# Performance work log

Measured on AMD Instinct MI355X. Metric: run time of the kernel, lower is better.

## Reference

```python
import jax, jax.numpy as jnp
import numpy as np

B, S, E, H, TOP = 256, 200, 64, 128, 200
LOC, T, N, HEADS, ALPHA = 50000, 168, 5000, 3, 0.2
NEG = -9e15


def _position_encoding(time_number, n_units, f=100.0):
    pos = np.arange(time_number, dtype=np.float32)
    unit = np.arange(n_units // 2, dtype=np.float32)
    rad = pos[None, :] / (f ** (unit[:, None] / (n_units // 2)))
    emb = np.concatenate([np.sin(rad), np.cos(rad)], axis=0)  # [n_units, T]
    return jnp.asarray(emb.T)  # [T, n_units]


def setup_inputs():
    key = jax.random.key(0)
    ks = jax.random.split(key, 24)
    inp = {}
    inp['u1'] = jax.random.randint(ks[0], (B,), 0, N)
    inp['u2'] = jax.random.randint(ks[1], (B,), 0, N)
    inp['length_1'] = jax.random.randint(ks[2], (B,), 2, S + 1)
    inp['length_2'] = jax.random.randint(ks[3], (B,), 2, S + 1)
    inp['loc_1'] = jax.random.randint(ks[4], (B, S), 0, LOC + 1)
    inp['loc_2'] = jax.random.randint(ks[5], (B, S), 0, LOC + 1)
    inp['time_1'] = jax.random.randint(ks[6], (B, S), 0, T)
    inp['time_2'] = jax.random.randint(ks[7], (B, S), 0, T)
    inp['time_gap_1'] = jax.random.uniform(ks[8], (B, S), jnp.float32) * 2.0
    inp['time_gap_2'] = jax.random.uniform(ks[9], (B, S), jnp.float32) * 2.0
    # parameters
    inp['loc_emb'] = jax.random.normal(ks[10], (LOC + 1, E), jnp.float32)
    inp['time_emb'] = _position_encoding(T, E, 100.0)  # frozen
    inp['user_emb'] = jax.random.normal(ks[11], (N, E), jnp.float32)
    g = 1.414 * jnp.sqrt(6.0 / (E + E))
    inp['gat_W'] = jax.random.uniform(ks[12], (HEADS, E, E), jnp.float32, -g, g)
    ga = 1.414 * jnp.sqrt(6.0 / (2 * E + 1))
    inp['gat_a'] = jax.random.uniform(ks[13], (HEADS, 2 * E, 1), jnp.float32, -ga, ga)
    inp['gat_Wout'] = jax.random.uniform(ks[14], (E, E), jnp.float32, -g, g)
    inp['gat_aout'] = jax.random.uniform(ks[15], (2 * E, 1), jnp.float32, -ga, ga)
    adj = (jax.random.uniform(ks[16], (N, N)) < 0.01).astype(jnp.float32)
    inp['adj'] = jnp.maximum(adj, jnp.eye(N, dtype=jnp.float32))
    s = 1.0 / jnp.sqrt(H)
    inp['Wih'] = jax.random.uniform(ks[17], (4 * H, E), jnp.float32, -s, s)
    inp['Whh'] = jax.random.uniform(ks[18], (4 * H, H), jnp.float32, -s, s)
    inp['bih'] = jax.random.uniform(ks[19], (4 * H,), jnp.float32, -s, s)
    inp['bhh'] = jax.random.uniform(ks[20], (4 * H,), jnp.float32, -s, s)
    inp['time_v'] = jax.random.uniform(ks[21], (H, 1), jnp.float32, -0.1, 0.1)
    inp['time_w'] = jnp.full((1, 1), 0.05, jnp.float32)
    inp['time_b'] = jnp.full((1, 1), 0.02, jnp.float32)
    fin = 2 * TOP + H + E
    sf = 1.0 / jnp.sqrt(fin)
    inp['fc_w'] = jax.random.uniform(ks[22], (2, fin), jnp.float32, -sf, sf)
    inp['fc_b'] = jax.random.uniform(ks[23], (2,), jnp.float32, -sf, sf)
    return inp


def _lstm(x, Wih, Whh, bih, bhh):
    # x: [B, S, E] -> hidden states [B, S, H], torch gate order i,f,g,o
    b = x.shape[0]
    xg = jnp.einsum('bse,ge->bsg', x, Wih) + bih + bhh  # [B,S,4H]

    def step(carry, xt):
        h, c = carry
        g = xt + h @ Whh.T
        i, f, gg, o = jnp.split(g, 4, axis=-1)
        c = jax.nn.sigmoid(f) * c + jax.nn.sigmoid(i) * jnp.tanh(gg)
        h = jax.nn.sigmoid(o) * jnp.tanh(c)
        return (h, c), h

    init = (jnp.zeros((b, H), x.dtype), jnp.zeros((b, H), x.dtype))
    _, hs = jax.lax.scan(step, init, xg.transpose(1, 0, 2))
    return hs.transpose(1, 0, 2)


def _gat_layer(x, W, a, adj):
    h = x @ W  # [N,F]
    F = h.shape[1]
    f1 = h @ a[:F, 0]  # [N]
    f2 = h @ a[F:, 0]  # [N]
    e = jax.nn.leaky_relu(f1[:, None] + f2[None, :], ALPHA)
    att = jnp.where(adj > 0, e, NEG)
    att = jax.nn.softmax(att, axis=1)
    return jax.nn.elu(att @ h)


def _gat(x, adj, gat_W, gat_a, gat_Wout, gat_aout):
    temp = jnp.zeros((x.shape[0], E), x.dtype)
    for i in range(HEADS):
        temp = temp + _gat_layer(x, gat_W[i], gat_a[i], adj)
    return _gat_layer(temp / HEADS, gat_Wout, gat_aout, adj)


def _time_loss(length, hidden, time_gap, time_v, time_w, time_b):
    tg = jnp.concatenate([time_gap[:, 1:], jnp.zeros((time_gap.shape[0], 1), time_gap.dtype)], axis=-1)
    p1 = jnp.einsum('bsh,h->bs', hidden, time_v[:, 0])
    w, bb = time_w[0, 0], time_b[0, 0]
    p2 = w * tg
    p3 = (1.0 / w) * jnp.exp(p1 + bb)
    p4 = (1.0 / w) * jnp.exp(p1 + p2 + bb)
    f1 = p1 + p2 + bb + p3 - p4  # [B,S]
    mask = jnp.arange(S)[None, :] < (length - 1)[:, None]
    per = jnp.sum(jnp.where(mask, f1, 0.0), axis=1) / (length - 1).astype(f1.dtype)
    return -jnp.mean(per)


def _masked_cos_vec(cos, length_1, length_2):
    # cos: [B,S,S]; row-max over valid cols, col-max over valid rows, zero-padded
    idx = jnp.arange(S)
    colm = idx[None, None, :] < length_2[:, None, None]
    rowm = idx[None, :, None] < length_1[:, None, None]
    hang = jnp.max(jnp.where(colm, cos, -jnp.inf), axis=2)  # [B,S]
    hang = jnp.where(idx[None, :] < length_1[:, None], hang, 0.0)
    lie = jnp.max(jnp.where(rowm, cos, -jnp.inf), axis=1)  # [B,S]
    lie = jnp.where(idx[None, :] < length_2[:, None], lie, 0.0)
    return jnp.concatenate([hang, lie], axis=1)  # [B, 2*TOP]


def reference(time_gap_1, time_gap_2, loc_emb, time_emb, user_emb, gat_W, gat_a,
              gat_Wout, gat_aout, adj, Wih, Whh, bih, bhh, time_v, time_w, time_b,
              fc_w, fc_b, u1, u2, length_1, length_2, loc_1, loc_2, time_1, time_2):
    # cosine-similarity matrix
    le1 = loc_emb[loc_1]  # [B,S,E]
    le2 = loc_emb[loc_2]
    n1 = jnp.sqrt(jnp.sum(le1 ** 2, axis=2))  # [B,S]
    n2 = jnp.sqrt(jnp.sum(le2 ** 2, axis=2))
    cos = jnp.einsum('bse,bte->bst', le1, le2) / (n1[:, :, None] * n2[:, None, :])
    matrix_ans = _masked_cos_vec(cos, length_1, length_2)

    # temporal LSTM branch (dropout inactive in eval)
    te1 = time_emb[time_1]
    te2 = time_emb[time_2]
    h1 = _lstm(te1, Wih, Whh, bih, bhh)
    h2 = _lstm(te2, Wih, Whh, bih, bhh)
    loss1 = _time_loss(length_1, h1, time_gap_1, time_v, time_w, time_b)
    loss2 = _time_loss(length_2, h2, time_gap_2, time_v, time_w, time_b)
    time_loss = loss1 + loss2

    bidx = jnp.arange(h1.shape[0])
    seq1 = h1[bidx, length_1 - 1]  # [B,H]
    seq2 = h2[bidx, length_2 - 1]
    time_ans = seq1 * seq2

    # GAT user embeddings (get_gat over full user graph)
    gat_embedding = _gat(user_emb, adj, gat_W, gat_a, gat_Wout, gat_aout)
    u_hadamard = gat_embedding[u1] * gat_embedding[u2]

    feat = jnp.concatenate([matrix_ans, jnp.tanh(time_ans), jnp.tanh(u_hadamard)], axis=1)
    outs = feat @ fc_w.T + fc_b
    return outs, time_loss
```

## Files before the change

### kernel.cpp

```cpp
#include <hip/hip_runtime.h>
#include <math.h>

#define Bb 256
#define Ss 200
#define Ee 64
#define Hh 128
#define Nn 5000
#define MAXN 160

__device__ __forceinline__ float wredsum(float v){
  #pragma unroll
  for (int o = 32; o; o >>= 1) v += __shfl_xor(v, o);
  return v;
}
__device__ __forceinline__ float wredmax(float v){
  #pragma unroll
  for (int o = 32; o; o >>= 1) v = fmaxf(v, __shfl_xor(v, o));
  return v;
}
__device__ __forceinline__ float sigf(float x){ return 1.f / (1.f + __expf(-x)); }
__device__ __forceinline__ float tanh_f(float x){
  float e = __expf(-2.f * fabsf(x));
  float t = (1.f - e) / (1.f + e);
  return copysignf(t, x);
}

__global__ void norm_gather(const float* __restrict__ loc_emb,
                            const int* __restrict__ loc1, const int* __restrict__ loc2,
                            float* __restrict__ ne1, float* __restrict__ ne2){
  int wid = blockIdx.x * 4 + (threadIdx.x >> 6);
  int lane = threadIdx.x & 63;
  const int total = Bb * Ss;
  if (wid >= 2 * total) return;
  const int* loc = (wid < total) ? loc1 : loc2;
  float* ne = (wid < total) ? ne1 : ne2;
  int r = (wid < total) ? wid : wid - total;
  int idx = loc[r];
  float v = loc_emb[(size_t)idx * Ee + lane];
  float ss = wredsum(v * v);
  ne[(size_t)r * Ee + lane] = v * rsqrtf(ss);
}

__global__ __launch_bounds__(256) void cosmax_kernel(const float* __restrict__ ne1,
                                                     const float* __restrict__ ne2,
                                                     const int* __restrict__ len1,
                                                     const int* __restrict__ len2,
                                                     float* __restrict__ matrix_ans){
  __shared__ __align__(16) float As[128][68];
  __shared__ __align__(16) float Bs[128][68];
  int b = blockIdx.x, tid = threadIdx.x;
  int tx = tid & 15, ty = tid >> 4;
  int L1 = len1[b], L2 = len2[b];
  const float4 zero4 = make_float4(0.f, 0.f, 0.f, 0.f);
  float lie[16];
  #pragma unroll
  for (int i = 0; i < 16; i++) lie[i] = -3.0e38f;

  for (int sc = 0; sc < 2; sc++){
    float hang[8];
    #pragma unroll
    for (int i = 0; i < 8; i++) hang[i] = -3.0e38f;
    __syncthreads();
    for (int i = tid; i < 2048; i += 256){
      int r = i >> 4, kq = i & 15;
      int row = sc * 128 + r;
      float4 v = (row < Ss) ? ((const float4*)ne1)[((size_t)b * Ss + row) * 16 + kq] : zero4;
      *(float4*)&As[r][kq * 4] = v;
    }
    for (int tc = 0; tc < 2; tc++){
      __syncthreads();
      for (int i = tid; i < 2048; i += 256){
        int r = i >> 4, kq = i & 15;
        int col = tc * 128 + r;
        float4 v = (col < Ss) ? ((const float4*)ne2)[((size_t)b * Ss + col) * 16 + kq] : zero4;
        *(float4*)&Bs[r][kq * 4] = v;
      }
      __syncthreads();
      float acc[8][8];
      #pragma unroll
      for (int i = 0; i < 8; i++)
        #pragma unroll
        for (int j = 0; j < 8; j++) acc[i][j] = 0.f;
      #pragma unroll 4
      for (int k4 = 0; k4 < 16; k4++){
        float4 a4[8], b4[8];
        #pragma unroll
        for (int i = 0; i < 8; i++) a4[i] = *(const float4*)&As[ty + 16 * i][k4 * 4];
        #pragma unroll
        for (int j = 0; j < 8; j++) b4[j] = *(const float4*)&Bs[tx + 16 * j][k4 * 4];
        #pragma unroll
        for (int i = 0; i < 8; i++)
          #pragma unroll
          for (int j = 0; j < 8; j++)
            acc[i][j] += a4[i].x * b4[j].x + a4[i].y * b4[j].y
                       + a4[i].z * b4[j].z + a4[i].w * b4[j].w;
      }
      #pragma unroll
      for (int j = 0; j < 8; j++){
        int col = tc * 128 + tx + 16 * j;
        bool cv = col < L2;
        #pragma unroll
        for (int i = 0; i < 8; i++){
          int row = sc * 128 + ty + 16 * i;
          float v = acc[i][j];
          if (cv) hang[i] = fmaxf(hang[i], v);
          if (row < L1) lie[tc * 8 + j] = fmaxf(lie[tc * 8 + j], v);
        }
      }
    }
    __syncthreads();
    float* fl = &As[0][0];
    #pragma unroll
    for (int i = 0; i < 8; i++) fl[(ty + 16 * i) * 16 + tx] = hang[i];
    __syncthreads();
    if (tid < 128){
      float m = -3.0e38f;
      #pragma unroll
      for (int p = 0; p < 16; p++) m = fmaxf(m, fl[tid * 16 + p]);
      int row = sc * 128 + tid;
      if (row < Ss) matrix_ans[(size_t)b * 400 + row] = (row < L1) ? m : 0.f;
    }
  }
  __syncthreads();
  float* fl = &As[0][0];
  #pragma unroll
  for (int i = 0; i < 16; i++){
    int tcc = i >> 3, j = i & 7;
    fl[(tcc * 128 + tx + 16 * j) * 16 + ty] = lie[i];
  }
  __syncthreads();
  {
    int t = tid;
    float m = -3.0e38f;
    #pragma unroll
    for (int p = 0; p < 16; p++) m = fmaxf(m, fl[t * 16 + p]);
    if (t < Ss) matrix_ans[(size_t)b * 400 + 200 + t] = (t < L2) ? m : 0.f;
  }
}

__global__ void xg_table(const float* __restrict__ time_emb, const float* __restrict__ Wih,
                         const float* __restrict__ bih, const float* __restrict__ bhh,
                         float* __restrict__ xgtab){
  int tt = blockIdx.x, g = threadIdx.x;
  __shared__ float xs[64];
  if (g < 64) xs[g] = time_emb[tt * 64 + g];
  __syncthreads();
  float acc = bih[g] + bhh[g];
  #pragma unroll
  for (int k = 0; k < 64; k++) acc += Wih[g * 64 + k] * xs[k];
  xgtab[tt * 512 + g] = acc;
}

__global__ __launch_bounds__(512) void lstm_kernel(const float* __restrict__ xgtab,
                                                   const int* __restrict__ time_1,
                                                   const int* __restrict__ time_2,
                                                   const float* __restrict__ Whh,
                                                   const float* __restrict__ tg1,
                                                   const float* __restrict__ tg2,
                                                   const int* __restrict__ len1,
                                                   const int* __restrict__ len2,
                                                   const float* __restrict__ time_v,
                                                   const float* __restrict__ time_w,
                                                   const float* __restrict__ time_b,
                                                   float* __restrict__ hfin1,
                                                   float* __restrict__ hfin2,
                                                   float* __restrict__ perb){
  int b = blockIdx.x, g = threadIdx.x;
  int lane = g & 63;
  __shared__ __align__(16) float h1s[128], h2s[128];
  __shared__ float g1s[512], g2s[512];
  __shared__ int t1s[Ss], t2s[Ss];
  __shared__ float tgs[2][Ss];
  __shared__ float red[4];
  float4 w4[32];
  #pragma unroll
  for (int k = 0; k < 32; k++) w4[k] = *(const float4*)(Whh + (size_t)g * 128 + k * 4);
  for (int i = g; i < Ss; i += 512){
    t1s[i] = time_1[b * Ss + i];
    t2s[i] = time_2[b * Ss + i];
    tgs[0][i] = (i < Ss - 1) ? tg1[b * Ss + i + 1] : 0.f;
    tgs[1][i] = (i < Ss - 1) ? tg2[b * Ss + i + 1] : 0.f;
  }
  if (g < 128){ h1s[g] = 0.f; h2s[g] = 0.f; }
  int l1 = len1[b], l2 = len2[b];
  float wv = time_w[0], bbias = time_b[0];
  float iw = 1.f / wv;
  float vd = (g < 256) ? time_v[g & 127] : 0.f;
  float lacc = 0.f;
  float c_reg = 0.f;
  __syncthreads();
  for (int t = 0; t < Ss; t++){
    float xg1 = xgtab[t1s[t] * 512 + g];
    float xg2 = xgtab[t2s[t] * 512 + g];
    float a1a = 0.f, a1b = 0.f, a2a = 0.f, a2b = 0.f;
    #pragma unroll
    for (int k = 0; k < 32; k += 2){
      float4 ha0 = *(const float4*)&h1s[k * 4];
      float4 hb0 = *(const float4*)&h2s[k * 4];
      float4 ha1 = *(const float4*)&h1s[k * 4 + 4];
      float4 hb1 = *(const float4*)&h2s[k * 4 + 4];
      a1a += w4[k].x * ha0.x + w4[k].y * ha0.y + w4[k].z * ha0.z + w4[k].w * ha0.w;
      a2a += w4[k].x * hb0.x + w4[k].y * hb0.y + w4[k].z * hb0.z + w4[k].w * hb0.w;
      a1b += w4[k+1].x * ha1.x + w4[k+1].y * ha1.y + w4[k+1].z * ha1.z + w4[k+1].w * ha1.w;
      a2b += w4[k+1].x * hb1.x + w4[k+1].y * hb1.y + w4[k+1].z * hb1.z + w4[k+1].w * hb1.w;
    }
    g1s[g] = a1a + a1b + xg1;
    g2s[g] = a2a + a2b + xg2;
    __syncthreads();
    if (g < 256){
      int d = g & 127;
      const float* gs = (g < 128) ? g1s : g2s;
      float ii = sigf(gs[d]);
      float ff = sigf(gs[128 + d]);
      float gg = tanh_f(gs[256 + d]);
      float oo = sigf(gs[384 + d]);
      float c = ff * c_reg + ii * gg;
      c_reg = c;
      float h = oo * tanh_f(c);
      if (g < 128){ h1s[d] = h; if (t == l1 - 1) hfin1[(size_t)b * 128 + d] = h; }
      else        { h2s[d] = h; if (t == l2 - 1) hfin2[(size_t)b * 128 + d] = h; }
      float r = wredsum(h * vd);
      if (lane == 0) red[g >> 6] = r;
    }
    __syncthreads();
    if (g < 2){
      float p = (g == 0) ? (red[0] + red[1]) : (red[2] + red[3]);
      int L = (g == 0) ? l1 : l2;
      if (t < L - 1){
        float p2 = wv * tgs[g][t];
        lacc += p + p2 + bbias + iw * expf(p + bbias) - iw * expf(p + p2 + bbias);
      }
    }
  }
  if (g < 2) red[g] = lacc;
  __syncthreads();
  if (g == 0) perb[b] = red[0] / (float)(l1 - 1) + red[1] / (float)(l2 - 1);
}

__global__ void build_csr(const float* __restrict__ adj, int* __restrict__ nbr, int* __restrict__ deg){
  int row = blockIdx.x * 4 + (threadIdx.x >> 6);
  int lane = threadIdx.x & 63;
  if (row >= Nn) return;
  const float* ar = adj + (size_t)row * Nn;
  int cnt = 0;
  for (int base = 0; base < Nn; base += 64){
    int c = base + lane;
    bool nz = (c < Nn) && (ar[c] > 0.f);
    unsigned long long m = __ballot(nz);
    if (nz){
      int pos = cnt + __popcll(m & ((1ULL << lane) - 1ULL));
      if (pos < MAXN) nbr[(size_t)row * MAXN + pos] = c;
    }
    cnt += __popcll(m);
  }
  if (lane == 0) deg[row] = (cnt > MAXN) ? MAXN : cnt;
}

__global__ __launch_bounds__(256) void gat_xw(const float* __restrict__ x, float scale,
                                              const float* __restrict__ W,
                                              const float* __restrict__ avec,
                                              float* __restrict__ hmat,
                                              float* __restrict__ f1, float* __restrict__ f2){
  __shared__ float Ws[64][64];
  __shared__ float as_[128];
  __shared__ float xs[4][64];
  int tid = threadIdx.x, lane = tid & 63, wid = tid >> 6;
  for (int i = tid; i < 4096; i += 256) Ws[i >> 6][i & 63] = W[i];
  if (tid < 128) as_[tid] = avec[tid];
  __syncthreads();
  int row = blockIdx.x * 4 + wid;
  xs[wid][lane] = x[(size_t)row * 64 + lane] * scale;
  float acc = 0.f;
  #pragma unroll
  for (int k = 0; k < 64; k++) acc += xs[wid][k] * Ws[k][lane];
  float p1 = wredsum(acc * as_[lane]);
  float p2 = wredsum(acc * as_[64 + lane]);
  hmat[(size_t)row * 64 + lane] = acc;
  if (lane == 0){ f1[row] = p1; f2[row] = p2; }
}

__global__ __launch_bounds__(256) void gat_att(const float* __restrict__ hmat,
                                               const float* __restrict__ f1,
                                               const float* __restrict__ f2,
                                               const int* __restrict__ nbr,
                                               const int* __restrict__ deg,
                                               float* __restrict__ outp, int accum){
  __shared__ int nbs[4][MAXN];
  __shared__ float attb[4][MAXN];
  int tid = threadIdx.x, lane = tid & 63, w = tid >> 6;
  int row = blockIdx.x * 4 + w;
  int d = deg[row];
  float fr = f1[row];
  float mx = -3.0e38f;
  for (int j = lane; j < d; j += 64){
    int c = nbr[(size_t)row * MAXN + j];
    nbs[w][j] = c;
    float e = fr + f2[c];
    e = (e >= 0.f) ? e : 0.2f * e;
    attb[w][j] = e;
    mx = fmaxf(mx, e);
  }
  mx = wredmax(mx);
  float sum = 0.f;
  for (int j = lane; j < d; j += 64){
    float ex = __expf(attb[w][j] - mx);
    attb[w][j] = ex;
    sum += ex;
  }
  sum = wredsum(sum);
  float inv = 1.f / sum;
  float acc = 0.f;
  for (int j = 0; j < d; j++)
    acc += attb[w][j] * hmat[(size_t)nbs[w][j] * 64 + lane];
  acc *= inv;
  acc = (acc > 0.f) ? acc : expm1f(acc);
  if (accum) outp[(size_t)row * 64 + lane] += acc;
  else       outp[(size_t)row * 64 + lane] = acc;
}

__global__ void final_fc(const float* __restrict__ matrix_ans,
                         const float* __restrict__ hfin1, const float* __restrict__ hfin2,
                         const float* __restrict__ gat_emb,
                         const int* __restrict__ u1, const int* __restrict__ u2,
                         const float* __restrict__ fc_w, const float* __restrict__ fc_b,
                         const float* __restrict__ perb, float* __restrict__ out){
  int b = blockIdx.x, lane = threadIdx.x;
  int a = u1[b], c = u2[b];
  float acc0 = 0.f, acc1 = 0.f;
  for (int i = lane; i < 592; i += 64){
    float f;
    if (i < 400) f = matrix_ans[(size_t)b * 400 + i];
    else if (i < 528){
      int d = i - 400;
      f = tanhf(hfin1[(size_t)b * 128 + d] * hfin2[(size_t)b * 128 + d]);
    } else {
      int d = i - 528;
      f = tanhf(gat_emb[(size_t)a * 64 + d] * gat_emb[(size_t)c * 64 + d]);
    }
    acc0 += f * fc_w[i];
    acc1 += f * fc_w[592 + i];
  }
  acc0 = wredsum(acc0);
  acc1 = wredsum(acc1);
  if (lane == 0){
    out[b * 2]     = acc0 + fc_b[0];
    out[b * 2 + 1] = acc1 + fc_b[1];
  }
  if (b == 0){
    float ls = 0.f;
    for (int i = lane; i < 256; i += 64) ls += perb[i];
    ls = wredsum(ls);
    if (lane == 0) out[512] = -ls / 256.f;
  }
}

extern "C" void kernel_launch(void* const* d_in, const int* in_sizes, int n_in,
                              void* d_out, int out_size, void* d_ws, size_t ws_size,
                              hipStream_t stream){
  (void)in_sizes; (void)n_in; (void)out_size; (void)ws_size;
  const int*   u1       = (const int*)  d_in[0];
  const int*   u2       = (const int*)  d_in[1];
  const int*   len1     = (const int*)  d_in[2];
  const int*   len2     = (const int*)  d_in[3];
  const int*   loc1     = (const int*)  d_in[4];
  const int*   loc2     = (const int*)  d_in[5];
  const int*   time1    = (const int*)  d_in[6];
  const int*   time2    = (const int*)  d_in[7];
  const float* tg1      = (const float*)d_in[8];
  const float* tg2      = (const float*)d_in[9];
  const float* loc_emb  = (const float*)d_in[10];
  const float* time_emb = (const float*)d_in[11];
  const float* user_emb = (const float*)d_in[12];
  const float* gat_W    = (const float*)d_in[13];
  const float* gat_a    = (const float*)d_in[14];
  const float* gat_Wout = (const float*)d_in[15];
  const float* gat_aout = (const float*)d_in[16];
  const float* adj      = (const float*)d_in[17];
  const float* Wih      = (const float*)d_in[18];
  const float* Whh      = (const float*)d_in[19];
  const float* bih      = (const float*)d_in[20];
  const float* bhh      = (const float*)d_in[21];
  const float* time_v   = (const float*)d_in[22];
  const float* time_w   = (const float*)d_in[23];
  const float* time_b   = (const float*)d_in[24];
  const float* fc_w     = (const float*)d_in[25];
  const float* fc_b     = (const float*)d_in[26];
  float* out = (float*)d_out;

  size_t off = 0;
  auto alloc = [&](size_t nbytes) -> void* {
    void* p = (char*)d_ws + off;
    off += (nbytes + 255) & ~(size_t)255;
    return p;
  };
  float* ne1        = (float*)alloc((size_t)Bb * Ss * Ee * 4);
  float* ne2        = (float*)alloc((size_t)Bb * Ss * Ee * 4);
  float* matrix_ans = (float*)alloc((size_t)Bb * 400 * 4);
  float* xgtab      = (float*)alloc((size_t)168 * 512 * 4);
  float* hfin1      = (float*)alloc((size_t)Bb * Hh * 4);
  float* hfin2      = (float*)alloc((size_t)Bb * Hh * 4);
  float* gat_h      = (float*)alloc((size_t)Nn * 64 * 4);
  float* gat_acc    = (float*)alloc((size_t)Nn * 64 * 4);
  float* gat_emb    = (float*)alloc((size_t)Nn * 64 * 4);
  float* f1w        = (float*)alloc((size_t)Nn * 4);
  float* f2w        = (float*)alloc((size_t)Nn * 4);
  float* perb       = (float*)alloc((size_t)Bb * 4);
  int*   nbr        = (int*)  alloc((size_t)Nn * MAXN * 4);
  int*   deg        = (int*)  alloc((size_t)Nn * 4);

  norm_gather<<<(2 * Bb * Ss) / 4, 256, 0, stream>>>(loc_emb, loc1, loc2, ne1, ne2);
  cosmax_kernel<<<Bb, 256, 0, stream>>>(ne1, ne2, len1, len2, matrix_ans);

  xg_table<<<168, 512, 0, stream>>>(time_emb, Wih, bih, bhh, xgtab);
  lstm_kernel<<<Bb, 512, 0, stream>>>(xgtab, time1, time2, Whh, tg1, tg2, len1, len2,
                                      time_v, time_w, time_b, hfin1, hfin2, perb);

  build_csr<<<Nn / 4, 256, 0, stream>>>(adj, nbr, deg);
  for (int hd = 0; hd < 3; hd++){
    gat_xw<<<Nn / 4, 256, 0, stream>>>(user_emb, 1.f, gat_W + (size_t)hd * 64 * 64,
                                       gat_a + (size_t)hd * 128, gat_h, f1w, f2w);
    gat_att<<<Nn / 4, 256, 0, stream>>>(gat_h, f1w, f2w, nbr, deg, gat_acc, hd == 0 ? 0 : 1);
  }
  gat_xw<<<Nn / 4, 256, 0, stream>>>(gat_acc, 1.f / 3.f, gat_Wout, gat_aout, gat_h, f1w, f2w);
  gat_att<<<Nn / 4, 256, 0, stream>>>(gat_h, f1w, f2w, nbr, deg, gat_emb, 0);

  final_fc<<<Bb, 64, 0, stream>>>(matrix_ans, hfin1, hfin2, gat_emb,
                                  u1, u2, fc_w, fc_b, perb, out);
}
```

Measured before the change: 909.6 us.

## Split LSTM recurrent matvec across lane quarters with 4 gates per thread

```diff
diff --git a/kernel.cpp b/kernel.cpp
--- a/kernel.cpp
+++ b/kernel.cpp
@@ -151,37 +151,43 @@
   xgtab[tt * 512 + g] = acc;
 }
 
-__global__ __launch_bounds__(512) void lstm_kernel(const float* __restrict__ xgtab,
-                                                   const int* __restrict__ time_1,
-                                                   const int* __restrict__ time_2,
-                                                   const float* __restrict__ Whh,
-                                                   const float* __restrict__ tg1,
-                                                   const float* __restrict__ tg2,
-                                                   const int* __restrict__ len1,
-                                                   const int* __restrict__ len2,
-                                                   const float* __restrict__ time_v,
-                                                   const float* __restrict__ time_w,
-                                                   const float* __restrict__ time_b,
-                                                   float* __restrict__ hfin1,
-                                                   float* __restrict__ hfin2,
-                                                   float* __restrict__ perb){
+#define HIDX(d) ((d) + (((d) >> 5) << 2))
+__global__ __launch_bounds__(512, 2) void lstm_kernel(const float* __restrict__ xgtab,
+                                                      const int* __restrict__ time_1,
+                                                      const int* __restrict__ time_2,
+                                                      const float* __restrict__ Whh,
+                                                      const float* __restrict__ tg1,
+                                                      const float* __restrict__ tg2,
+                                                      const int* __restrict__ len1,
+                                                      const int* __restrict__ len2,
+                                                      const float* __restrict__ time_v,
+                                                      const float* __restrict__ time_w,
+                                                      const float* __restrict__ time_b,
+                                                      float* __restrict__ hfin1,
+                                                      float* __restrict__ hfin2,
+                                                      float* __restrict__ perb){
   int b = blockIdx.x, g = threadIdx.x;
-  int lane = g & 63;
-  __shared__ __align__(16) float h1s[128], h2s[128];
-  __shared__ float g1s[512], g2s[512];
+  int lane = g & 63, wave = g >> 6;
+  int kq = lane >> 4;
+  int g0 = (wave * 16 + (lane & 15)) * 4;
+  __shared__ __align__(16) float h1s[144], h2s[144];
+  __shared__ __align__(16) float g1s[512], g2s[512];
   __shared__ int t1s[Ss], t2s[Ss];
   __shared__ float tgs[2][Ss];
   __shared__ float red[4];
-  float4 w4[32];
-  #pragma unroll
-  for (int k = 0; k < 32; k++) w4[k] = *(const float4*)(Whh + (size_t)g * 128 + k * 4);
+  float4 w4[4][8];
+  #pragma unroll
+  for (int j = 0; j < 4; j++)
+    #pragma unroll
+    for (int q = 0; q < 8; q++)
+      w4[j][q] = *(const float4*)(Whh + (size_t)(g0 + j) * 128 + kq * 32 + q * 4);
   for (int i = g; i < Ss; i += 512){
     t1s[i] = time_1[b * Ss + i];
     t2s[i] = time_2[b * Ss + i];
     tgs[0][i] = (i < Ss - 1) ? tg1[b * Ss + i + 1] : 0.f;
     tgs[1][i] = (i < Ss - 1) ? tg2[b * Ss + i + 1] : 0.f;
   }
-  if (g < 128){ h1s[g] = 0.f; h2s[g] = 0.f; }
+  if (g < 144){ h1s[g] = 0.f; h2s[g] = 0.f; }
   int l1 = len1[b], l2 = len2[b];
   float wv = time_w[0], bbias = time_b[0];
   float iw = 1.f / wv;
@@ -190,22 +196,36 @@
   float c_reg = 0.f;
   __syncthreads();
   for (int t = 0; t < Ss; t++){
-    float xg1 = xgtab[t1s[t] * 512 + g];
-    float xg2 = xgtab[t2s[t] * 512 + g];
-    float a1a = 0.f, a1b = 0.f, a2a = 0.f, a2b = 0.f;
-    #pragma unroll
-    for (int k = 0; k < 32; k += 2){
-      float4 ha0 = *(const float4*)&h1s[k * 4];
-      float4 hb0 = *(const float4*)&h2s[k * 4];
-      float4 ha1 = *(const float4*)&h1s[k * 4 + 4];
-      float4 hb1 = *(const float4*)&h2s[k * 4 + 4];
-      a1a += w4[k].x * ha0.x + w4[k].y * ha0.y + w4[k].z * ha0.z + w4[k].w * ha0.w;
-      a2a += w4[k].x * hb0.x + w4[k].y * hb0.y + w4[k].z * hb0.z + w4[k].w * hb0.w;
-      a1b += w4[k+1].x * ha1.x + w4[k+1].y * ha1.y + w4[k+1].z * ha1.z + w4[k+1].w * ha1.w;
-      a2b += w4[k+1].x * hb1.x + w4[k+1].y * hb1.y + w4[k+1].z * hb1.z + w4[k+1].w * hb1.w;
-    }
-    g1s[g] = a1a + a1b + xg1;
-    g2s[g] = a2a + a2b + xg2;
+    float4 xg1, xg2;
+    if (kq == 0){
+      xg1 = *(const float4*)(xgtab + (size_t)t1s[t] * 512 + g0);
+      xg2 = *(const float4*)(xgtab + (size_t)t2s[t] * 512 + g0);
+    }
+    float a1[4] = {0.f, 0.f, 0.f, 0.f};
+    float a2[4] = {0.f, 0.f, 0.f, 0.f};
+    const float4* hp1 = (const float4*)&h1s[kq * 36];
+    const float4* hp2 = (const float4*)&h2s[kq * 36];
+    #pragma unroll
+    for (int q = 0; q < 8; q++){
+      float4 hv1 = hp1[q];
+      float4 hv2 = hp2[q];
+      #pragma unroll
+      for (int j = 0; j < 4; j++){
+        a1[j] += w4[j][q].x * hv1.x + w4[j][q].y * hv1.y + w4[j][q].z * hv1.z + w4[j][q].w * hv1.w;
+        a2[j] += w4[j][q].x * hv2.x + w4[j][q].y * hv2.y + w4[j][q].z * hv2.z + w4[j][q].w * hv2.w;
+      }
+    }
+    #pragma unroll
+    for (int j = 0; j < 4; j++){
+      a1[j] += __shfl_xor(a1[j], 16); a1[j] += __shfl_xor(a1[j], 32);
+      a2[j] += __shfl_xor(a2[j], 16); a2[j] += __shfl_xor(a2[j], 32);
+    }
+    if (kq == 0){
+      float4 o1 = make_float4(a1[0] + xg1.x, a1[1] + xg1.y, a1[2] + xg1.z, a1[3] + xg1.w);
+      float4 o2 = make_float4(a2[0] + xg2.x, a2[1] + xg2.y, a2[2] + xg2.z, a2[3] + xg2.w);
+      *(float4*)&g1s[g0] = o1;
+      *(float4*)&g2s[g0] = o2;
+    }
     __syncthreads();
     if (g < 256){
       int d = g & 127;
@@ -217,8 +237,8 @@
       float c = ff * c_reg + ii * gg;
       c_reg = c;
       float h = oo * tanh_f(c);
-      if (g < 128){ h1s[d] = h; if (t == l1 - 1) hfin1[(size_t)b * 128 + d] = h; }
-      else        { h2s[d] = h; if (t == l2 - 1) hfin2[(size_t)b * 128 + d] = h; }
+      if (g < 128){ h1s[HIDX(d)] = h; if (t == l1 - 1) hfin1[(size_t)b * 128 + d] = h; }
+      else        { h2s[HIDX(d)] = h; if (t == l2 - 1) hfin2[(size_t)b * 128 + d] = h; }
       float r = wredsum(h * vd);
       if (lane == 0) red[g >> 6] = r;
     }
```

Result: faster. 765.1 us (-15.9%).
